# Performance work log

Hardware: AMD Instinct MI355X
Metric: run time of the kernel (lower is better)

Reference implementation:

```python
import jax, jax.numpy as jnp
import numpy as np

N_NODES = 100000
N_EDGES = 1600000
IN_C = 128
HID = 128
OUT_C = 16
BN_EPS = 1e-5


def _uniform(key, shape, fan_in):
    lim = 1.0 / np.sqrt(fan_in)
    return jax.random.uniform(key, shape, jnp.float32, -lim, lim)


def setup_inputs() -> dict:
    key = jax.random.key(0)
    ks = jax.random.split(key, 24)
    inp = {
        "x": jax.random.normal(ks[0], (N_NODES, IN_C), jnp.float32),
        "edge_index": jax.random.randint(ks[1], (2, N_EDGES), 0, N_NODES, dtype=jnp.int32),
    }
    dims = [(IN_C, HID), (HID, HID), (HID, OUT_C)]
    for l, (fi, fo) in enumerate(dims):
        inp[f"Wn{l}"] = _uniform(ks[2 + 3 * l], (fi, fo), fi)   # lin_l (neighbor) weight
        inp[f"b{l}"] = _uniform(ks[3 + 3 * l], (fo,), fi)        # lin_l bias
        inp[f"Ws{l}"] = _uniform(ks[4 + 3 * l], (fi, fo), fi)   # lin_r (self/root) weight, no bias
    for l in range(2):  # BatchNorm params for the first num_layers-1 layers (eval mode)
        inp[f"g{l}"] = jnp.ones((HID,), jnp.float32)
        inp[f"be{l}"] = jnp.zeros((HID,), jnp.float32)
        inp[f"rm{l}"] = jax.random.normal(ks[12 + 2 * l], (HID,), jnp.float32) * 0.1
        inp[f"rv{l}"] = jax.random.uniform(ks[13 + 2 * l], (HID,), jnp.float32, 0.5, 1.5)
    return inp


def _sage_conv(h, src, dst, Wn, b, Ws):
    # PyG SAGEConv (aggr='mean'): out = lin_l(mean_{j in N(i)} x_j) + lin_r(x_i)
    n = h.shape[0]
    msg = h[src]                                                   # [E, F] gather
    s = jax.ops.segment_sum(msg, dst, num_segments=n)              # [N, F]
    cnt = jax.ops.segment_sum(jnp.ones((src.shape[0], 1), h.dtype), dst, num_segments=n)
    agg = s / jnp.maximum(cnt, 1.0)                                # mean over neighbors
    return agg @ Wn + b + h @ Ws


def _bn_eval(h, g, be, rm, rv):
    return (h - rm) * jax.lax.rsqrt(rv + BN_EPS) * g + be


def reference(x, edge_index, Wn0, b0, Ws0, Wn1, b1, Ws1, Wn2, b2, Ws2,
              g0, be0, rm0, rv0, g1, be1, rm1, rv1):
    src, dst = edge_index[0], edge_index[1]
    h = _sage_conv(x, src, dst, Wn0, b0, Ws0)
    h = jax.nn.relu(_bn_eval(h, g0, be0, rm0, rv0))   # eval: dropout is identity
    h = _sage_conv(h, src, dst, Wn1, b1, Ws1)
    h = jax.nn.relu(_bn_eval(h, g1, be1, rm1, rv1))
    return _sage_conv(h, src, dst, Wn2, b2, Ws2)
```

## Files before the change

kernel.cpp:

```cpp
#include <hip/hip_runtime.h>
#include <hip/hip_bf16.h>


constexpr int N   = 100000;
constexpr int E   = 1600000;
constexpr int F   = 128;
constexpr int FO  = 16;
constexpr int CAP = 64;

constexpr int GEMM_BLOCKS = (N + 63) / 64;
constexpr int FILL_BLOCKS = 1042;
constexpr int FUSED_GRID  = GEMM_BLOCKS + FILL_BLOCKS;

typedef __attribute__((ext_vector_type(8))) short bf16x8;
typedef __attribute__((ext_vector_type(4))) float f32x4;

__device__ __forceinline__ ushort f2bf(float v) {
  return __bfloat16_as_ushort(__float2bfloat16(v));
}
__device__ __forceinline__ float bf2f(ushort u) {
  return __uint_as_float(((unsigned)u) << 16);
}
__device__ __forceinline__ float bf_lo(unsigned u) {
  return __uint_as_float(u << 16);
}
__device__ __forceinline__ float bf_hi(unsigned u) {
  return __uint_as_float(u & 0xffff0000u);
}

__global__ void pack2_k(const float* __restrict__ Wn0, const float* __restrict__ Ws0,
                        const float* __restrict__ Wn1, const float* __restrict__ Ws1,
                        ushort* __restrict__ Bt0, ushort* __restrict__ Bt1) {
  int t = blockIdx.x * blockDim.x + threadIdx.x;
  int which = t >> 15;
  int i = t & 32767;
  int n = i >> 7;
  int k = i & 127;
  const float* Wn = which ? Wn1 : Wn0;
  const float* Ws = which ? Ws1 : Ws0;
  ushort* Bt = which ? Bt1 : Bt0;
  float w = (n < 128) ? Wn[k * F + n] : Ws[k * F + (n - 128)];
  Bt[i] = f2bf(w);
}

__device__ __forceinline__ void gemm_body(
    int bg, int tid,
    const float* __restrict__ h_in, const ushort* __restrict__ Bt,
    const float* __restrict__ b,
    ushort* __restrict__ y, float* __restrict__ s,
    char* Ahi, char* Alo) {
  const int row0 = bg * 64;

#pragma unroll
  for (int j = 0; j < 4; ++j) {
    int f = tid + j * 256;
    int row = f >> 4;
    int kc = f & 15;
    int gr = row0 + row; if (gr >= N) gr = N - 1;
    const float4* gp = reinterpret_cast<const float4*>(h_in + (size_t)gr * F + kc * 8);
    float4 v0 = gp[0], v1 = gp[1];
    float vv[8] = {v0.x, v0.y, v0.z, v0.w, v1.x, v1.y, v1.z, v1.w};
    unsigned ph[4], pl[4];
#pragma unroll
    for (int q = 0; q < 4; ++q) {
      ushort h0 = f2bf(vv[2 * q]);
      ushort h1 = f2bf(vv[2 * q + 1]);
      ushort l0 = f2bf(vv[2 * q] - bf2f(h0));
      ushort l1 = f2bf(vv[2 * q + 1] - bf2f(h1));
      ph[q] = (unsigned)h0 | ((unsigned)h1 << 16);
      pl[q] = (unsigned)l0 | ((unsigned)l1 << 16);
    }
    int off = (row * 256 + kc * 16) ^ ((row & 7) << 4);
    *reinterpret_cast<uint4*>(Ahi + off) = make_uint4(ph[0], ph[1], ph[2], ph[3]);
    *reinterpret_cast<uint4*>(Alo + off) = make_uint4(pl[0], pl[1], pl[2], pl[3]);
  }
  __syncthreads();

  const int lane = tid & 63;
  const int wave = tid >> 6;
  const int wcol0 = wave * 64;
  const int lg = lane >> 4;
  const int lr = lane & 15;

  f32x4 acc[4][4];
#pragma unroll
  for (int r = 0; r < 4; ++r)
#pragma unroll
    for (int c = 0; c < 4; ++c) acc[r][c] = f32x4{0.f, 0.f, 0.f, 0.f};

#pragma unroll
  for (int kk = 0; kk < 4; ++kk) {
    bf16x8 bfr[4];
#pragma unroll
    for (int c = 0; c < 4; ++c) {
      int col = wcol0 + c * 16 + lr;
      bfr[c] = *reinterpret_cast<const bf16x8*>(Bt + (size_t)col * F + kk * 32 + lg * 8);
    }
#pragma unroll
    for (int r = 0; r < 4; ++r) {
      int row = r * 16 + lr;
      int off = (row * 256 + kk * 64 + lg * 16) ^ ((row & 7) << 4);
      bf16x8 a = *reinterpret_cast<const bf16x8*>(Ahi + off);
#pragma unroll
      for (int c = 0; c < 4; ++c)
        acc[r][c] = __builtin_amdgcn_mfma_f32_16x16x32_bf16(a, bfr[c], acc[r][c], 0, 0, 0);
    }
#pragma unroll
    for (int r = 0; r < 4; ++r) {
      int row = r * 16 + lr;
      int off = (row * 256 + kk * 64 + lg * 16) ^ ((row & 7) << 4);
      bf16x8 a = *reinterpret_cast<const bf16x8*>(Alo + off);
#pragma unroll
      for (int c = 0; c < 4; ++c)
        acc[r][c] = __builtin_amdgcn_mfma_f32_16x16x32_bf16(a, bfr[c], acc[r][c], 0, 0, 0);
    }
  }

  if (wave < 2) {
#pragma unroll
    for (int r = 0; r < 4; ++r)
#pragma unroll
      for (int c = 0; c < 4; ++c) {
        int col = wcol0 + c * 16 + lr;
#pragma unroll
        for (int q = 0; q < 4; ++q) {
          int grow = row0 + r * 16 + lg * 4 + q;
          if (grow < N) y[(size_t)grow * F + col] = f2bf(acc[r][c][q]);
        }
      }
  } else {
#pragma unroll
    for (int r = 0; r < 4; ++r)
#pragma unroll
      for (int c = 0; c < 4; ++c) {
        int scol = wcol0 - 128 + c * 16 + lr;
        float bias = b[scol];
#pragma unroll
        for (int q = 0; q < 4; ++q) {
          int grow = row0 + r * 16 + lg * 4 + q;
          if (grow < N) s[(size_t)grow * F + scol] = acc[r][c][q] + bias;
        }
      }
  }
}

__global__ __launch_bounds__(256) void fused0_k(
    const float* __restrict__ x, const ushort* __restrict__ Bt0,
    const float* __restrict__ b0,
    ushort* __restrict__ y, float* __restrict__ s,
    const int* __restrict__ src, const int* __restrict__ dst,
    int* __restrict__ degc, int* __restrict__ slots) {
  __shared__ uint4 AsU[2048];
  char* Ahi = reinterpret_cast<char*>(AsU);
  char* Alo = Ahi + 64 * 256;
  const int gid = blockIdx.x;
  const int grp = gid / 5, rem = gid % 5;
  const int tid = threadIdx.x;

  if (rem < 3) {
    gemm_body(grp * 3 + rem, tid, x, Bt0, b0, y, s, Ahi, Alo);
  } else {
    const int bf = grp * 2 + (rem - 3);
    int i = bf * 256 + tid;
    const int stride = FILL_BLOCKS * 256;
    for (; i < E; i += stride) {
      int d = dst[i];
      int pos = atomicAdd(&degc[d], 1);
      if (pos < CAP)
        __builtin_nontemporal_store(src[i], &slots[(size_t)d * CAP + pos]);
    }
  }
}

__global__ __launch_bounds__(256) void dual_gemm_mfma_k(
    const float* __restrict__ h_in, const ushort* __restrict__ Bt,
    const float* __restrict__ b,
    ushort* __restrict__ y, float* __restrict__ s) {
  __shared__ uint4 AsU[2048];
  char* Ahi = reinterpret_cast<char*>(AsU);
  char* Alo = Ahi + 64 * 256;
  gemm_body(blockIdx.x, threadIdx.x, h_in, Bt, b, y, s, Ahi, Alo);
}

__global__ __launch_bounds__(256) void agg_epi_k(
    const int* __restrict__ degc, const int* __restrict__ slots,
    const ushort* __restrict__ y, const float* __restrict__ s,
    const float* __restrict__ g, const float* __restrict__ be,
    const float* __restrict__ rm, const float* __restrict__ rv,
    float* __restrict__ h_out) {
  const int node = blockIdx.x * 4 + (threadIdx.x >> 6);
  const int c2 = threadIdx.x & 63;
  int deg = degc[node]; if (deg > CAP) deg = CAP;
  const int* sl = slots + (size_t)node * CAP;

  float a0 = 0.f, a1 = 0.f, a2 = 0.f, a3 = 0.f;
  float b0 = 0.f, b1 = 0.f, b2 = 0.f, b3 = 0.f;
  int e = 0;
  for (; e + 4 <= deg; e += 4) {
    int n0 = sl[e], n1 = sl[e + 1], n2 = sl[e + 2], n3 = sl[e + 3];
    unsigned u0 = *reinterpret_cast<const unsigned*>(y + (size_t)n0 * F + c2 * 2);
    unsigned u1 = *reinterpret_cast<const unsigned*>(y + (size_t)n1 * F + c2 * 2);
    unsigned u2 = *reinterpret_cast<const unsigned*>(y + (size_t)n2 * F + c2 * 2);
    unsigned u3 = *reinterpret_cast<const unsigned*>(y + (size_t)n3 * F + c2 * 2);
    a0 += bf_lo(u0); b0 += bf_hi(u0);
    a1 += bf_lo(u1); b1 += bf_hi(u1);
    a2 += bf_lo(u2); b2 += bf_hi(u2);
    a3 += bf_lo(u3); b3 += bf_hi(u3);
  }
  for (; e < deg; ++e) {
    unsigned u = *reinterpret_cast<const unsigned*>(y + (size_t)sl[e] * F + c2 * 2);
    a0 += bf_lo(u); b0 += bf_hi(u);
  }
  const float inv = 1.0f / fmaxf((float)deg, 1.0f);
  const float mlo = ((a0 + a1) + (a2 + a3)) * inv;
  const float mhi = ((b0 + b1) + (b2 + b3)) * inv;

  const int cA = 2 * c2;
  float2 sv = *reinterpret_cast<const float2*>(s + (size_t)node * F + cA);
  float2 gv = *reinterpret_cast<const float2*>(g + cA);
  float2 bev = *reinterpret_cast<const float2*>(be + cA);
  float2 rmv = *reinterpret_cast<const float2*>(rm + cA);
  float2 rvv = *reinterpret_cast<const float2*>(rv + cA);
  float olo = (mlo + sv.x - rmv.x) * (rsqrtf(rvv.x + 1e-5f) * gv.x) + bev.x;
  float ohi = (mhi + sv.y - rmv.y) * (rsqrtf(rvv.y + 1e-5f) * gv.y) + bev.y;
  float2 o = make_float2(fmaxf(olo, 0.f), fmaxf(ohi, 0.f));
  *reinterpret_cast<float2*>(h_out + (size_t)node * F + cA) = o;
}

__global__ __launch_bounds__(256) void gemm2_k(
    const float* __restrict__ h_in,
    const float* __restrict__ Wn, const float* __restrict__ Ws,
    const float* __restrict__ b,
    ushort* __restrict__ y2, float* __restrict__ s2) {
  __shared__ float hL[16][F];
  const int tid = threadIdx.x;
  const int row0 = blockIdx.x * 16;
#pragma unroll
  for (int j = 0; j < 2; ++j) {
    int f = tid + j * 256;
    int r = f >> 5;
    int cc = f & 31;
    reinterpret_cast<float4*>(&hL[r][0])[cc] =
        reinterpret_cast<const float4*>(h_in + (size_t)(row0 + r) * F)[cc];
  }
  __syncthreads();

  const int c = tid & 15;
  const int r = tid >> 4;
  float ay = 0.f, as = 0.f;
  for (int k0 = 0; k0 < F; k0 += 4) {
    float4 hv = *reinterpret_cast<const float4*>(&hL[r][k0]);
    ay += hv.x * Wn[(k0 + 0) * FO + c] + hv.y * Wn[(k0 + 1) * FO + c]
        + hv.z * Wn[(k0 + 2) * FO + c] + hv.w * Wn[(k0 + 3) * FO + c];
    as += hv.x * Ws[(k0 + 0) * FO + c] + hv.y * Ws[(k0 + 1) * FO + c]
        + hv.z * Ws[(k0 + 2) * FO + c] + hv.w * Ws[(k0 + 3) * FO + c];
  }
  y2[(size_t)(row0 + r) * FO + c] = f2bf(ay);
  s2[(size_t)(row0 + r) * FO + c] = as + b[c];
}

__global__ __launch_bounds__(256) void agg_out_k(
    const int* __restrict__ degc, const int* __restrict__ slots,
    const ushort* __restrict__ y2, const float* __restrict__ s2,
    float* __restrict__ out) {
  const int node = blockIdx.x * 4 + (threadIdx.x >> 6);
  const int lane = threadIdx.x & 63;
  const int c = lane & 15;
  const int j = lane >> 4;
  int deg = degc[node]; if (deg > CAP) deg = CAP;
  const int* sl = slots + (size_t)node * CAP;
  float acc = 0.f;
  for (int e = j; e < deg; e += 4) {
    unsigned bits = y2[(size_t)sl[e] * FO + c];
    acc += __uint_as_float(bits << 16);
  }
  acc += __shfl_xor(acc, 16, 64);
  acc += __shfl_xor(acc, 32, 64);
  if (j == 0)
    out[(size_t)node * FO + c] = acc / fmaxf((float)deg, 1.0f) + s2[(size_t)node * FO + c];
}

extern "C" void kernel_launch(void* const* d_in, const int* in_sizes, int n_in,
                              void* d_out, int out_size, void* d_ws, size_t ws_size,
                              hipStream_t stream) {
  const float* x   = (const float*)d_in[0];
  const int*   ei  = (const int*)d_in[1];
  const float* Wn0 = (const float*)d_in[2];
  const float* b0  = (const float*)d_in[3];
  const float* Ws0 = (const float*)d_in[4];
  const float* Wn1 = (const float*)d_in[5];
  const float* b1  = (const float*)d_in[6];
  const float* Ws1 = (const float*)d_in[7];
  const float* Wn2 = (const float*)d_in[8];
  const float* b2  = (const float*)d_in[9];
  const float* Ws2 = (const float*)d_in[10];
  const float* g0  = (const float*)d_in[11];
  const float* be0 = (const float*)d_in[12];
  const float* rm0 = (const float*)d_in[13];
  const float* rv0 = (const float*)d_in[14];
  const float* g1  = (const float*)d_in[15];
  const float* be1 = (const float*)d_in[16];
  const float* rm1 = (const float*)d_in[17];
  const float* rv1 = (const float*)d_in[18];

  const int* src = ei;
  const int* dst = ei + E;

  int* degc    = (int*)d_ws;
  int* slots   = degc + N;
  ushort* y    = (ushort*)(slots + (size_t)N * CAP);
  float* s     = (float*)(y + (size_t)N * F);
  float* h     = s + (size_t)N * F;
  ushort* Bt0  = (ushort*)(h + (size_t)N * F);
  ushort* Bt1  = Bt0 + 256 * 128;
  ushort* y2   = y;
  float* s2    = s;

  hipMemsetAsync(degc, 0, N * sizeof(int), stream);
  pack2_k<<<256, 256, 0, stream>>>(Wn0, Ws0, Wn1, Ws1, Bt0, Bt1);

  fused0_k<<<FUSED_GRID, 256, 0, stream>>>(x, Bt0, b0, y, s, src, dst, degc, slots);
  agg_epi_k<<<N / 4, 256, 0, stream>>>(degc, slots, y, s, g0, be0, rm0, rv0, h);

  dual_gemm_mfma_k<<<GEMM_BLOCKS, 256, 0, stream>>>(h, Bt1, b1, y, s);
  agg_epi_k<<<N / 4, 256, 0, stream>>>(degc, slots, y, s, g1, be1, rm1, rv1, h);

  gemm2_k<<<N / 16, 256, 0, stream>>>(h, Wn2, Ws2, b2, y2, s2);
  agg_out_k<<<N / 4, 256, 0, stream>>>(degc, slots, y2, s2, (float*)d_out);
}
```

Baseline: 510.6 us.

## Fuse neighbor aggregation and BN epilogue into next layer's MFMA GEMM

The mean-aggregation, BatchNorm and ReLU epilogue of layers 0 and 1 now run inside the next layer's GEMM kernel. Each block gathers 64 nodes, splits the results into hi/lo bf16 and writes them straight into LDS for the MFMA, so the fp32 hidden activations no longer round-trip through global memory. The final 128-to-16 projection also moves from a scalar FMA kernel to MFMA using a third packed bf16 weight buffer. In exchange, the latency-bound gather now runs with far fewer blocks, 16 sequential node rounds per wave and 32KB of LDS per block, which may hide gather latency less well.

Measured after the change: 633.4 us. 1.24x slower.

```diff
diff --git a/kernel.cpp b/kernel.cpp
--- a/kernel.cpp
+++ b/kernel.cpp
@@ -28,29 +28,56 @@
   return __uint_as_float(u & 0xffff0000u);
 }
 
-__global__ void pack2_k(const float* __restrict__ Wn0, const float* __restrict__ Ws0,
+__global__ void pack3_k(const float* __restrict__ Wn0, const float* __restrict__ Ws0,
                         const float* __restrict__ Wn1, const float* __restrict__ Ws1,
-                        ushort* __restrict__ Bt0, ushort* __restrict__ Bt1) {
+                        const float* __restrict__ Wn2, const float* __restrict__ Ws2,
+                        ushort* __restrict__ Bt0, ushort* __restrict__ Bt1,
+                        ushort* __restrict__ Bt2) {
   int t = blockIdx.x * blockDim.x + threadIdx.x;
-  int which = t >> 15;
-  int i = t & 32767;
-  int n = i >> 7;
-  int k = i & 127;
-  const float* Wn = which ? Wn1 : Wn0;
-  const float* Ws = which ? Ws1 : Ws0;
-  ushort* Bt = which ? Bt1 : Bt0;
-  float w = (n < 128) ? Wn[k * F + n] : Ws[k * F + (n - 128)];
-  Bt[i] = f2bf(w);
-}
-
-__device__ __forceinline__ void gemm_body(
-    int bg, int tid,
-    const float* __restrict__ h_in, const ushort* __restrict__ Bt,
-    const float* __restrict__ b,
-    ushort* __restrict__ y, float* __restrict__ s,
-    char* Ahi, char* Alo) {
-  const int row0 = bg * 64;
-
+  if (t < 65536) {
+    int which = t >> 15;
+    int i = t & 32767;
+    int n = i >> 7, k = i & 127;
+    const float* Wn = which ? Wn1 : Wn0;
+    const float* Ws = which ? Ws1 : Ws0;
+    float w = (n < 128) ? Wn[k * F + n] : Ws[k * F + (n - 128)];
+    (which ? Bt1 : Bt0)[i] = f2bf(w);
+  } else if (t < 65536 + 4096) {
+    int i = t - 65536;
+    int n = i >> 7, k = i & 127;
+    float w = (n < FO) ? Wn2[k * FO + n] : Ws2[k * FO + (n - FO)];
+    Bt2[i] = f2bf(w);
+  }
+}
+
+__device__ __forceinline__ void gather_mean(
+    const int* __restrict__ sl, int deg, const ushort* __restrict__ ybuf,
+    int c2, float& mlo, float& mhi) {
+  float a0 = 0.f, a1 = 0.f, a2 = 0.f, a3 = 0.f;
+  float b0 = 0.f, b1 = 0.f, b2 = 0.f, b3 = 0.f;
+  int e = 0;
+  for (; e + 4 <= deg; e += 4) {
+    int n0 = sl[e], n1 = sl[e + 1], n2 = sl[e + 2], n3 = sl[e + 3];
+    unsigned u0 = *reinterpret_cast<const unsigned*>(ybuf + (size_t)n0 * F + c2 * 2);
+    unsigned u1 = *reinterpret_cast<const unsigned*>(ybuf + (size_t)n1 * F + c2 * 2);
+    unsigned u2 = *reinterpret_cast<const unsigned*>(ybuf + (size_t)n2 * F + c2 * 2);
+    unsigned u3 = *reinterpret_cast<const unsigned*>(ybuf + (size_t)n3 * F + c2 * 2);
+    a0 += bf_lo(u0); b0 += bf_hi(u0);
+    a1 += bf_lo(u1); b1 += bf_hi(u1);
+    a2 += bf_lo(u2); b2 += bf_hi(u2);
+    a3 += bf_lo(u3); b3 += bf_hi(u3);
+  }
+  for (; e < deg; ++e) {
+    unsigned u = *reinterpret_cast<const unsigned*>(ybuf + (size_t)sl[e] * F + c2 * 2);
+    a0 += bf_lo(u); b0 += bf_hi(u);
+  }
+  const float inv = 1.0f / fmaxf((float)deg, 1.0f);
+  mlo = ((a0 + a1) + (a2 + a3)) * inv;
+  mhi = ((b0 + b1) + (b2 + b3)) * inv;
+}
+
+__device__ __forceinline__ void gemm_stage_from_global(
+    int row0, int tid, const float* __restrict__ h_in, char* Ahi, char* Alo) {
 #pragma unroll
   for (int j = 0; j < 4; ++j) {
     int f = tid + j * 256;
@@ -74,8 +101,11 @@
     *reinterpret_cast<uint4*>(Ahi + off) = make_uint4(ph[0], ph[1], ph[2], ph[3]);
     *reinterpret_cast<uint4*>(Alo + off) = make_uint4(pl[0], pl[1], pl[2], pl[3]);
   }
-  __syncthreads();
-
+}
+
+__device__ __forceinline__ void gemm_mfma_256(
+    int row0, int tid, const ushort* __restrict__ Bt, const float* __restrict__ b,
+    ushort* __restrict__ y, float* __restrict__ s, char* Ahi, char* Alo) {
   const int lane = tid & 63;
   const int wave = tid >> 6;
   const int wcol0 = wave * 64;
@@ -158,7 +188,10 @@
   const int tid = threadIdx.x;
 
   if (rem < 3) {
-    gemm_body(grp * 3 + rem, tid, x, Bt0, b0, y, s, Ahi, Alo);
+    int bg = grp * 3 + rem;
+    gemm_stage_from_global(bg * 64, tid, x, Ahi, Alo);
+    __syncthreads();
+    gemm_mfma_256(bg * 64, tid, Bt0, b0, y, s, Ahi, Alo);
   } else {
     const int bf = grp * 2 + (rem - 3);
     int i = bf * 256 + tid;
@@ -172,91 +205,140 @@
   }
 }
 
-__global__ __launch_bounds__(256) void dual_gemm_mfma_k(
-    const float* __restrict__ h_in, const ushort* __restrict__ Bt,
-    const float* __restrict__ b,
-    ushort* __restrict__ y, float* __restrict__ s) {
+__global__ __launch_bounds__(256) void fused1_k(
+    const int* __restrict__ degc, const int* __restrict__ slots,
+    const ushort* __restrict__ yA, float* __restrict__ s,
+    const float* __restrict__ g, const float* __restrict__ be,
+    const float* __restrict__ rm, const float* __restrict__ rv,
+    const ushort* __restrict__ Bt1, const float* __restrict__ b1,
+    ushort* __restrict__ yB) {
   __shared__ uint4 AsU[2048];
   char* Ahi = reinterpret_cast<char*>(AsU);
   char* Alo = Ahi + 64 * 256;
-  gemm_body(blockIdx.x, threadIdx.x, h_in, Bt, b, y, s, Ahi, Alo);
-}
-
-__global__ __launch_bounds__(256) void agg_epi_k(
-    const int* __restrict__ degc, const int* __restrict__ slots,
-    const ushort* __restrict__ y, const float* __restrict__ s,
-    const float* __restrict__ g, const float* __restrict__ be,
-    const float* __restrict__ rm, const float* __restrict__ rv,
-    float* __restrict__ h_out) {
-  const int node = blockIdx.x * 4 + (threadIdx.x >> 6);
-  const int c2 = threadIdx.x & 63;
-  int deg = degc[node]; if (deg > CAP) deg = CAP;
-  const int* sl = slots + (size_t)node * CAP;
-
-  float a0 = 0.f, a1 = 0.f, a2 = 0.f, a3 = 0.f;
-  float b0 = 0.f, b1 = 0.f, b2 = 0.f, b3 = 0.f;
-  int e = 0;
-  for (; e + 4 <= deg; e += 4) {
-    int n0 = sl[e], n1 = sl[e + 1], n2 = sl[e + 2], n3 = sl[e + 3];
-    unsigned u0 = *reinterpret_cast<const unsigned*>(y + (size_t)n0 * F + c2 * 2);
-    unsigned u1 = *reinterpret_cast<const unsigned*>(y + (size_t)n1 * F + c2 * 2);
-    unsigned u2 = *reinterpret_cast<const unsigned*>(y + (size_t)n2 * F + c2 * 2);
-    unsigned u3 = *reinterpret_cast<const unsigned*>(y + (size_t)n3 * F + c2 * 2);
-    a0 += bf_lo(u0); b0 += bf_hi(u0);
-    a1 += bf_lo(u1); b1 += bf_hi(u1);
-    a2 += bf_lo(u2); b2 += bf_hi(u2);
-    a3 += bf_lo(u3); b3 += bf_hi(u3);
-  }
-  for (; e < deg; ++e) {
-    unsigned u = *reinterpret_cast<const unsigned*>(y + (size_t)sl[e] * F + c2 * 2);
-    a0 += bf_lo(u); b0 += bf_hi(u);
-  }
-  const float inv = 1.0f / fmaxf((float)deg, 1.0f);
-  const float mlo = ((a0 + a1) + (a2 + a3)) * inv;
-  const float mhi = ((b0 + b1) + (b2 + b3)) * inv;
-
-  const int cA = 2 * c2;
-  float2 sv = *reinterpret_cast<const float2*>(s + (size_t)node * F + cA);
+  const int tid = threadIdx.x;
+  const int row0 = blockIdx.x * 64;
+  const int nd = tid >> 6;
+  const int c2 = tid & 63;
+  const int cA = c2 * 2;
+
   float2 gv = *reinterpret_cast<const float2*>(g + cA);
   float2 bev = *reinterpret_cast<const float2*>(be + cA);
   float2 rmv = *reinterpret_cast<const float2*>(rm + cA);
   float2 rvv = *reinterpret_cast<const float2*>(rv + cA);
-  float olo = (mlo + sv.x - rmv.x) * (rsqrtf(rvv.x + 1e-5f) * gv.x) + bev.x;
-  float ohi = (mhi + sv.y - rmv.y) * (rsqrtf(rvv.y + 1e-5f) * gv.y) + bev.y;
-  float2 o = make_float2(fmaxf(olo, 0.f), fmaxf(ohi, 0.f));
-  *reinterpret_cast<float2*>(h_out + (size_t)node * F + cA) = o;
-}
-
-__global__ __launch_bounds__(256) void gemm2_k(
-    const float* __restrict__ h_in,
-    const float* __restrict__ Wn, const float* __restrict__ Ws,
-    const float* __restrict__ b,
+  const float sc0 = rsqrtf(rvv.x + 1e-5f) * gv.x;
+  const float sc1 = rsqrtf(rvv.y + 1e-5f) * gv.y;
+
+#pragma unroll 1
+  for (int round = 0; round < 16; ++round) {
+    int row = round * 4 + nd;
+    int node = row0 + row;
+    int nc = node < N ? node : N - 1;
+    int deg = degc[nc]; if (deg > CAP) deg = CAP;
+    float mlo, mhi;
+    gather_mean(slots + (size_t)nc * CAP, deg, yA, c2, mlo, mhi);
+    float2 sv = *reinterpret_cast<const float2*>(s + (size_t)nc * F + cA);
+    float olo = fmaxf((mlo + sv.x - rmv.x) * sc0 + bev.x, 0.f);
+    float ohi = fmaxf((mhi + sv.y - rmv.y) * sc1 + bev.y, 0.f);
+    ushort h0 = f2bf(olo), l0 = f2bf(olo - bf2f(h0));
+    ushort h1 = f2bf(ohi), l1 = f2bf(ohi - bf2f(h1));
+    int off = (row * 256 + c2 * 4) ^ ((row & 7) << 4);
+    *reinterpret_cast<unsigned*>(Ahi + off) = (unsigned)h0 | ((unsigned)h1 << 16);
+    *reinterpret_cast<unsigned*>(Alo + off) = (unsigned)l0 | ((unsigned)l1 << 16);
+  }
+  __syncthreads();
+  gemm_mfma_256(row0, tid, Bt1, b1, yB, s, Ahi, Alo);
+}
+
+__global__ __launch_bounds__(256) void fused2_k(
+    const int* __restrict__ degc, const int* __restrict__ slots,
+    const ushort* __restrict__ yB, const float* __restrict__ s,
+    const float* __restrict__ g, const float* __restrict__ be,
+    const float* __restrict__ rm, const float* __restrict__ rv,
+    const ushort* __restrict__ Bt2, const float* __restrict__ b2,
     ushort* __restrict__ y2, float* __restrict__ s2) {
-  __shared__ float hL[16][F];
+  __shared__ uint4 AsU[2048];
+  char* Ahi = reinterpret_cast<char*>(AsU);
+  char* Alo = Ahi + 64 * 256;
   const int tid = threadIdx.x;
-  const int row0 = blockIdx.x * 16;
-#pragma unroll
-  for (int j = 0; j < 2; ++j) {
-    int f = tid + j * 256;
-    int r = f >> 5;
-    int cc = f & 31;
-    reinterpret_cast<float4*>(&hL[r][0])[cc] =
-        reinterpret_cast<const float4*>(h_in + (size_t)(row0 + r) * F)[cc];
+  const int row0 = blockIdx.x * 64;
+  const int nd = tid >> 6;
+  const int c2 = tid & 63;
+  const int cA = c2 * 2;
+
+  float2 gv = *reinterpret_cast<const float2*>(g + cA);
+  float2 bev = *reinterpret_cast<const float2*>(be + cA);
+  float2 rmv = *reinterpret_cast<const float2*>(rm + cA);
+  float2 rvv = *reinterpret_cast<const float2*>(rv + cA);
+  const float sc0 = rsqrtf(rvv.x + 1e-5f) * gv.x;
+  const float sc1 = rsqrtf(rvv.y + 1e-5f) * gv.y;
+
+#pragma unroll 1
+  for (int round = 0; round < 16; ++round) {
+    int row = round * 4 + nd;
+    int node = row0 + row;
+    int nc = node < N ? node : N - 1;
+    int deg = degc[nc]; if (deg > CAP) deg = CAP;
+    float mlo, mhi;
+    gather_mean(slots + (size_t)nc * CAP, deg, yB, c2, mlo, mhi);
+    float2 sv = *reinterpret_cast<const float2*>(s + (size_t)nc * F + cA);
+    float olo = fmaxf((mlo + sv.x - rmv.x) * sc0 + bev.x, 0.f);
+    float ohi = fmaxf((mhi + sv.y - rmv.y) * sc1 + bev.y, 0.f);
+    ushort h0 = f2bf(olo), l0 = f2bf(olo - bf2f(h0));
+    ushort h1 = f2bf(ohi), l1 = f2bf(ohi - bf2f(h1));
+    int off = (row * 256 + c2 * 4) ^ ((row & 7) << 4);
+    *reinterpret_cast<unsigned*>(Ahi + off) = (unsigned)h0 | ((unsigned)h1 << 16);
+    *reinterpret_cast<unsigned*>(Alo + off) = (unsigned)l0 | ((unsigned)l1 << 16);
   }
   __syncthreads();
 
-  const int c = tid & 15;
-  const int r = tid >> 4;
-  float ay = 0.f, as = 0.f;
-  for (int k0 = 0; k0 < F; k0 += 4) {
-    float4 hv = *reinterpret_cast<const float4*>(&hL[r][k0]);
-    ay += hv.x * Wn[(k0 + 0) * FO + c] + hv.y * Wn[(k0 + 1) * FO + c]
-        + hv.z * Wn[(k0 + 2) * FO + c] + hv.w * Wn[(k0 + 3) * FO + c];
-    as += hv.x * Ws[(k0 + 0) * FO + c] + hv.y * Ws[(k0 + 1) * FO + c]
-        + hv.z * Ws[(k0 + 2) * FO + c] + hv.w * Ws[(k0 + 3) * FO + c];
-  }
-  y2[(size_t)(row0 + r) * FO + c] = f2bf(ay);
-  s2[(size_t)(row0 + r) * FO + c] = as + b[c];
+  const int lane = tid & 63;
+  const int wave = tid >> 6;
+  if (wave >= 2) return;
+  const int lg = lane >> 4;
+  const int lr = lane & 15;
+  const int col = wave * 16 + lr;
+
+  f32x4 acc[4];
+#pragma unroll
+  for (int r = 0; r < 4; ++r) acc[r] = f32x4{0.f, 0.f, 0.f, 0.f};
+
+#pragma unroll
+  for (int kk = 0; kk < 4; ++kk) {
+    bf16x8 bfr = *reinterpret_cast<const bf16x8*>(Bt2 + (size_t)col * F + kk * 32 + lg * 8);
+#pragma unroll
+    for (int r = 0; r < 4; ++r) {
+      int row = r * 16 + lr;
+      int off = (row * 256 + kk * 64 + lg * 16) ^ ((row & 7) << 4);
+      bf16x8 a = *reinterpret_cast<const bf16x8*>(Ahi + off);
+      acc[r] = __builtin_amdgcn_mfma_f32_16x16x32_bf16(a, bfr, acc[r], 0, 0, 0);
+    }
+#pragma unroll
+    for (int r = 0; r < 4; ++r) {
+      int row = r * 16 + lr;
+      int off = (row * 256 + kk * 64 + lg * 16) ^ ((row & 7) << 4);
+      bf16x8 a = *reinterpret_cast<const bf16x8*>(Alo + off);
+      acc[r] = __builtin_amdgcn_mfma_f32_16x16x32_bf16(a, bfr, acc[r], 0, 0, 0);
+    }
+  }
+
+  if (wave == 0) {
+#pragma unroll
+    for (int r = 0; r < 4; ++r)
+#pragma unroll
+      for (int q = 0; q < 4; ++q) {
+        int grow = row0 + r * 16 + lg * 4 + q;
+        if (grow < N) y2[(size_t)grow * FO + lr] = f2bf(acc[r][q]);
+      }
+  } else {
+    float bias = b2[lr];
+#pragma unroll
+    for (int r = 0; r < 4; ++r)
+#pragma unroll
+      for (int q = 0; q < 4; ++q) {
+        int grow = row0 + r * 16 + lg * 4 + q;
+        if (grow < N) s2[(size_t)grow * FO + lr] = acc[r][q] + bias;
+      }
+  }
 }
 
 __global__ __launch_bounds__(256) void agg_out_k(
@@ -308,23 +390,25 @@
 
   int* degc    = (int*)d_ws;
   int* slots   = degc + N;
-  ushort* y    = (ushort*)(slots + (size_t)N * CAP);
-  float* s     = (float*)(y + (size_t)N * F);
-  float* h     = s + (size_t)N * F;
-  ushort* Bt0  = (ushort*)(h + (size_t)N * F);
+  ushort* yA   = (ushort*)(slots + (size_t)N * CAP);
+  float* s     = (float*)(yA + (size_t)N * F);
+  ushort* yB   = (ushort*)(s + (size_t)N * F);
+  ushort* Bt0  = yB + (size_t)N * F;
   ushort* Bt1  = Bt0 + 256 * 128;
-  ushort* y2   = y;
-  float* s2    = s;
+  ushort* Bt2  = Bt1 + 256 * 128;
+  ushort* y2   = yA;
+  float*  s2   = (float*)(yA + (size_t)N * FO);
 
   hipMemsetAsync(degc, 0, N * sizeof(int), stream);
-  pack2_k<<<256, 256, 0, stream>>>(Wn0, Ws0, Wn1, Ws1, Bt0, Bt1);
-
-  fused0_k<<<FUSED_GRID, 256, 0, stream>>>(x, Bt0, b0, y, s, src, dst, degc, slots);
-  agg_epi_k<<<N / 4, 256, 0, stream>>>(degc, slots, y, s, g0, be0, rm0, rv0, h);
-
-  dual_gemm_mfma_k<<<GEMM_BLOCKS, 256, 0, stream>>>(h, Bt1, b1, y, s);
-  agg_epi_k<<<N / 4, 256, 0, stream>>>(degc, slots, y, s, g1, be1, rm1, rv1, h);
-
-  gemm2_k<<<N / 16, 256, 0, stream>>>(h, Wn2, Ws2, b2, y2, s2);
+  pack3_k<<<273, 256, 0, stream>>>(Wn0, Ws0, Wn1, Ws1, Wn2, Ws2, Bt0, Bt1, Bt2);
+
+  fused0_k<<<FUSED_GRID, 256, 0, stream>>>(x, Bt0, b0, yA, s, src, dst, degc, slots);
+
+  fused1_k<<<GEMM_BLOCKS, 256, 0, stream>>>(degc, slots, yA, s,
+                                            g0, be0, rm0, rv0, Bt1, b1, yB);
+
+  fused2_k<<<GEMM_BLOCKS, 256, 0, stream>>>(degc, slots, yB, s,
+                                            g1, be1, rm1, rv1, Bt2, b2, y2, s2);
+
   agg_out_k<<<N / 4, 256, 0, stream>>>(degc, slots, y2, s2, (float*)d_out);
 }
```
